# Kernel tuning notes

Hardware: AMD Instinct MI355X
Metric: run time of the kernel (lower is better)

Reference implementation:

```python
import jax, jax.numpy as jnp
import numpy as np

B, T, C, H = 4, 2048, 1024, 16


def setup_inputs() -> dict:
    key = jax.random.key(0)
    ks = jax.random.split(key, 8)
    s = 0.02
    return {
        "xq": jax.random.normal(ks[0], (B, T, C), jnp.float32),
        "xk": jax.random.normal(ks[1], (B, T, C), jnp.float32),
        "xv": jax.random.normal(ks[2], (B, T, C), jnp.float32),
        "Wq": jax.random.normal(ks[3], (C, C), jnp.float32) * s,
        "Wk": jax.random.normal(ks[4], (C, C), jnp.float32) * s,
        "Wv": jax.random.normal(ks[5], (C, C), jnp.float32) * s,
        "Wo": jax.random.normal(ks[6], (C, C), jnp.float32) * s,
        "bo": jnp.zeros((C,), jnp.float32),
    }


def reference(xq, xk, xv, Wq, Wk, Wv, Wo, bo):
    # torch nn.Linear: y = x @ W.T
    q = xq @ Wq.T  # (B,T,C)
    k = xk @ Wk.T
    v = xv @ Wv.T
    hd = C // H
    # (B,T,C) -> (B,H,T,hd)
    q = q.reshape(B, T, H, hd).transpose(0, 2, 1, 3)
    k = k.reshape(B, T, H, hd).transpose(0, 2, 1, 3)
    v = v.reshape(B, T, H, hd).transpose(0, 2, 1, 3)
    scale = 1.0 / jnp.sqrt(jnp.asarray(hd, q.dtype))
    att = jnp.einsum("bhqd,bhkd->bhqk", q, k) * scale  # (B,H,T,T)
    causal = jnp.tril(jnp.ones((T, T), bool))
    att = jnp.where(causal, att, jnp.asarray(-jnp.inf, att.dtype))
    att = jax.nn.softmax(att, axis=-1)
    y = jnp.einsum("bhqk,bhkd->bhqd", att, v)  # (B,H,T,hd)
    y = y.transpose(0, 2, 1, 3).reshape(B, T, C)
    return y @ Wo.T + bo
```

## Files before the change

### kernel.cpp

```cpp
#include <hip/hip_runtime.h>
#include <stdint.h>

#define B_ 4
#define T_ 2048
#define C_ 1024
#define H_ 16
#define HD 64

typedef __attribute__((ext_vector_type(8))) short bf16x8;
typedef __attribute__((ext_vector_type(4))) short bf16x4;
typedef __attribute__((ext_vector_type(4))) float v4f;
typedef __attribute__((ext_vector_type(4))) uint32_t v4u;

static __device__ __forceinline__ short f2bf(float f) {
    union { float f; uint32_t u; } v; v.f = f;
    uint32_t u = v.u;
    uint32_t r = (u + 0x7fffu + ((u >> 16) & 1u)) >> 16;
    return (short)(r & 0xffffu);
}
static __device__ __forceinline__ uint32_t pack2(float x, float y) {
    uint32_t a = __float_as_uint(x) + 0x8000u;
    uint32_t b = __float_as_uint(y) + 0x8000u;
    return __builtin_amdgcn_perm(b, a, 0x07060302u);
}
static __device__ __forceinline__ uint32_t pack2t(float x, float y) {
    return __builtin_amdgcn_perm(__float_as_uint(y), __float_as_uint(x), 0x07060302u);
}
static __device__ __forceinline__ void gload_lds16(const void* g, void* l) {
    __builtin_amdgcn_global_load_lds(
        (const __attribute__((address_space(1))) void*)g,
        (__attribute__((address_space(3))) void*)l, 16, 0, 0);
}

__global__ __launch_bounds__(256) void convw(
    const float* __restrict__ w0, const float* __restrict__ w1,
    const float* __restrict__ w2, const float* __restrict__ w3,
    short* __restrict__ out)
{
    const float* src = (blockIdx.y == 0) ? w0 : (blockIdx.y == 1) ? w1 :
                       (blockIdx.y == 2) ? w2 : w3;
    short* dst = out + (size_t)blockIdx.y * (C_ * C_);
    int id = blockIdx.x * 256 + threadIdx.x;
    const float* p = src + (size_t)id * 8;
    v4f a0 = *(const v4f*)p, a1 = *(const v4f*)(p + 4);
    v4u dv;
    dv[0] = pack2(a0[0], a0[1]); dv[1] = pack2(a0[2], a0[3]);
    dv[2] = pack2(a1[0], a1[1]); dv[3] = pack2(a1[2], a1[3]);
    *(v4u*)&dst[(size_t)id * 8] = dv;
}

template <int MODE>
__global__ __launch_bounds__(256) void gemm_nt(
    const void* A0, const void* A1,
    const void* B0, const void* B1,
    void* O0, void* O1,
    const float* __restrict__ bias, float s0, float s1)
{
    const void* Aptr = blockIdx.z ? A1 : A0;
    const void* Bptr = blockIdx.z ? B1 : B0;
    void* Out = blockIdx.z ? O1 : O0;
    const float oscale = blockIdx.z ? s1 : s0;

    const int K = 1024;
    __shared__ short As[128 * 32];
    __shared__ short Bs[128 * 32];
    const int t = threadIdx.x;
    const int w = t >> 6, l = t & 63, g = l >> 4, c = l & 15;
    const int wm = w & 1, wn = w >> 1;
    const int m0 = blockIdx.x * 128, n0 = blockIdx.y * 128;

    v4f acc[4][4];
#pragma unroll
    for (int i = 0; i < 4; ++i)
#pragma unroll
        for (int j = 0; j < 4; ++j) acc[i][j] = (v4f){0.f, 0.f, 0.f, 0.f};

    for (int k0 = 0; k0 < K; k0 += 32) {
        __syncthreads();
        if (MODE != 0) {
            const short* Ab = (const short*)Aptr;
#pragma unroll
            for (int i = 0; i < 2; ++i) {
                int cb = w * 2 + i;
                const short* gp = Ab + (size_t)(m0 + cb * 16 + (l >> 2)) * K + k0 + (l & 3) * 8;
                gload_lds16(gp, &As[cb * 512]);
            }
        }
        if (MODE != 1) {
            const short* Bb = (const short*)Bptr;
#pragma unroll
            for (int i = 0; i < 2; ++i) {
                int cb = w * 2 + i;
                const short* gp = Bb + (size_t)(n0 + cb * 16 + (l >> 2)) * K + k0 + (l & 3) * 8;
                gload_lds16(gp, &Bs[cb * 512]);
            }
        }
        if (MODE == 0) {
            const float* Af = (const float*)Aptr;
#pragma unroll
            for (int i = 0; i < 2; ++i) {
                int id = i * 256 + t;
                const float* p = Af + (size_t)(m0 + (id >> 2)) * K + k0 + (id & 3) * 8;
                v4f a0 = *(const v4f*)p, a1 = *(const v4f*)(p + 4);
                v4u dv;
                dv[0] = pack2(a0[0], a0[1]); dv[1] = pack2(a0[2], a0[3]);
                dv[2] = pack2(a1[0], a1[1]); dv[3] = pack2(a1[2], a1[3]);
                *(v4u*)&As[id * 8] = dv;
            }
        }
        if (MODE == 1) {
            const float* Bf = (const float*)Bptr;
#pragma unroll
            for (int i = 0; i < 2; ++i) {
                int id = i * 256 + t;
                const float* p = Bf + (size_t)(n0 + (id >> 2)) * K + k0 + (id & 3) * 8;
                v4f a0 = *(const v4f*)p, a1 = *(const v4f*)(p + 4);
                v4u dv;
                dv[0] = pack2(a0[0], a0[1]); dv[1] = pack2(a0[2], a0[3]);
                dv[2] = pack2(a1[0], a1[1]); dv[3] = pack2(a1[2], a1[3]);
                *(v4u*)&Bs[id * 8] = dv;
            }
        }
        __syncthreads();
        bf16x8 af[4], bfr[4];
#pragma unroll
        for (int i = 0; i < 4; ++i)
            af[i] = *(const bf16x8*)&As[(wm * 64 + i * 16 + c) * 32 + g * 8];
#pragma unroll
        for (int j = 0; j < 4; ++j)
            bfr[j] = *(const bf16x8*)&Bs[(wn * 64 + j * 16 + c) * 32 + g * 8];
#pragma unroll
        for (int i = 0; i < 4; ++i)
#pragma unroll
            for (int j = 0; j < 4; ++j)
                acc[i][j] = __builtin_amdgcn_mfma_f32_16x16x32_bf16(af[i], bfr[j], acc[i][j], 0, 0, 0);
    }
#pragma unroll
    for (int i = 0; i < 4; ++i)
#pragma unroll
        for (int j = 0; j < 4; ++j)
#pragma unroll
            for (int r = 0; r < 4; ++r) {
                int m = m0 + wm * 64 + i * 16 + g * 4 + r;
                int n = n0 + wn * 64 + j * 16 + c;
                float vv = acc[i][j][r];
                if (MODE == 2) {
                    ((float*)Out)[(size_t)m * C_ + n] = vv + bias[n];
                } else if (MODE == 0) {
                    int b = m >> 11, tt = m & (T_ - 1);
                    int h = n >> 6, d = n & 63;
                    ((short*)Out)[((size_t)(b * H_ + h) * T_ + tt) * HD + d] = f2bf(vv * oscale);
                } else {
                    int b = n >> 11, tt = n & (T_ - 1);
                    int h = m >> 6, d = m & 63;
                    ((short*)Out)[((size_t)(b * H_ + h) * HD + d) * T_ + tt] = f2bf(vv);
                }
            }
}

__global__ __launch_bounds__(256) void attn_kernel(
    const short* __restrict__ Q, const short* __restrict__ Kp,
    const short* __restrict__ Vt, short* __restrict__ Y)
{
    __shared__ short Ks[2 * 64 * 32];
    __shared__ short Vs[64 * 72];
    const int t = threadIdx.x;
    const int w = t >> 6, l = t & 63, g = l >> 4, c = l & 15;
    const int bid = blockIdx.x;
    const int slot = bid >> 3;
    const int p = slot & 15;
    const size_t bh = (size_t)((bid & 7) * 8 + (slot >> 4));

    bf16x8 ones;
#pragma unroll
    for (int i = 0; i < 8; ++i) ones[i] = (short)0x3F80;

    for (int qi = 0; qi < 2; ++qi) {
        const int qt = qi ? (31 - p) : p;
        const int qbase = qt * 64;

        bf16x8 qf0, qf1;
        {
            const short* qp = &Q[(bh * T_ + qbase + w * 16 + c) * HD + g * 8];
            qf0 = *(const bf16x8*)qp;
            qf1 = *(const bf16x8*)(qp + 32);
        }

        v4f O[4], accl;
        accl = (v4f){0.f, 0.f, 0.f, 0.f};
#pragma unroll
        for (int d = 0; d < 4; ++d) O[d] = (v4f){0.f, 0.f, 0.f, 0.f};

        for (int kb = 0; kb <= qt; ++kb) {
            const int kbase = kb * 64;
            __syncthreads();
#pragma unroll
            for (int i = 0; i < 2; ++i) {
                int gi = w * 2 + i;
                int hk = gi >> 2, rb = gi & 3;
                const short* gp = &Kp[(bh * T_ + kbase + rb * 16 + (l >> 2)) * HD + hk * 32 + (l & 3) * 8];
                gload_lds16(gp, &Ks[hk * 2048 + rb * 512]);
            }
#pragma unroll
            for (int i = 0; i < 2; ++i) {
                int id = i * 256 + t;
                int rr = id >> 3, cc = id & 7;
                *(bf16x8*)&Vs[rr * 72 + cc * 8] =
                    *(const bf16x8*)&Vt[(bh * HD + rr) * T_ + kbase + cc * 8];
            }
            __syncthreads();

            float s2[4][4];
#pragma unroll
            for (int j = 0; j < 4; ++j) {
                bf16x8 kf0 = *(const bf16x8*)&Ks[(j * 16 + c) * 32 + g * 8];
                bf16x8 kf1 = *(const bf16x8*)&Ks[2048 + (j * 16 + c) * 32 + g * 8];
                v4f sa = (v4f){0.f, 0.f, 0.f, 0.f};
                sa = __builtin_amdgcn_mfma_f32_16x16x32_bf16(kf0, qf0, sa, 0, 0, 0);
                sa = __builtin_amdgcn_mfma_f32_16x16x32_bf16(kf1, qf1, sa, 0, 0, 0);
#pragma unroll
                for (int r = 0; r < 4; ++r) s2[j][r] = sa[r];
            }
            if (kb == qt) {
                const int q = qbase + w * 16 + c;
#pragma unroll
                for (int j = 0; j < 4; ++j)
#pragma unroll
                    for (int r = 0; r < 4; ++r) {
                        int key = kbase + j * 16 + g * 4 + r;
                        if (key > q) s2[j][r] = -3.0e38f;
                    }
            }
            union { bf16x8 v; uint32_t u[4]; } pa[2];
#pragma unroll
            for (int s = 0; s < 2; ++s)
#pragma unroll
                for (int wi = 0; wi < 4; ++wi) {
                    int j = 2 * s + (wi >> 1);
                    int r0 = (wi & 1) * 2;
                    float x = __builtin_amdgcn_exp2f(s2[j][r0]);
                    float y = __builtin_amdgcn_exp2f(s2[j][r0 + 1]);
                    pa[s].u[wi] = pack2t(x, y);
                }
#pragma unroll
            for (int s = 0; s < 2; ++s) {
                bf16x8 af = pa[s].v;
#pragma unroll
                for (int d = 0; d < 4; ++d) {
                    const short* vp = &Vs[(d * 16 + c) * 72 + s * 32 + g * 4];
                    union { bf16x8 v8; bf16x4 v4[2]; } vu;
                    vu.v4[0] = *(const bf16x4*)vp;
                    vu.v4[1] = *(const bf16x4*)(vp + 16);
                    O[d] = __builtin_amdgcn_mfma_f32_16x16x32_bf16(af, vu.v8, O[d], 0, 0, 0);
                }
                accl = __builtin_amdgcn_mfma_f32_16x16x32_bf16(af, ones, accl, 0, 0, 0);
            }
        }
#pragma unroll
        for (int r = 0; r < 4; ++r) {
            float rl = 1.0f / accl[r];
            size_t rowoff = ((size_t)(bh >> 4) * T_ + qbase + w * 16 + g * 4 + r) * C_ + (bh & 15) * HD;
#pragma unroll
            for (int d = 0; d < 4; ++d)
                Y[rowoff + d * 16 + c] = f2bf(O[d][r] * rl);
        }
    }
}

extern "C" void kernel_launch(void* const* d_in, const int* in_sizes, int n_in,
                              void* d_out, int out_size, void* d_ws, size_t ws_size,
                              hipStream_t stream) {
    const float* xq = (const float*)d_in[0];
    const float* xk = (const float*)d_in[1];
    const float* xv = (const float*)d_in[2];
    const float* Wq = (const float*)d_in[3];
    const float* Wk = (const float*)d_in[4];
    const float* Wv = (const float*)d_in[5];
    const float* Wo = (const float*)d_in[6];
    const float* bo = (const float*)d_in[7];

    const size_t NE = (size_t)B_ * H_ * T_ * HD;
    const size_t WE = (size_t)C_ * C_;
    short* Qh  = (short*)d_ws;
    short* Kh  = Qh + NE;
    short* Vt  = Kh + NE;
    short* Y   = Vt + NE;
    short* Wbf = Y + NE;

    const float qscale = 0.18033688011112042f;
    dim3 blk(256);

    hipLaunchKernelGGL(convw, dim3(512, 4), blk, 0, stream, Wq, Wk, Wv, Wo, Wbf);
    hipLaunchKernelGGL((gemm_nt<0>), dim3(64, 8, 2), blk, 0, stream,
                       (const void*)xq, (const void*)xk,
                       (const void*)(Wbf + 0 * WE), (const void*)(Wbf + 1 * WE),
                       (void*)Qh, (void*)Kh, (const float*)nullptr, qscale, 1.0f);
    hipLaunchKernelGGL((gemm_nt<1>), dim3(8, 64, 1), blk, 0, stream,
                       (const void*)(Wbf + 2 * WE), (const void*)(Wbf + 2 * WE),
                       (const void*)xv, (const void*)xv,
                       (void*)Vt, (void*)Vt, (const float*)nullptr, 1.0f, 1.0f);
    hipLaunchKernelGGL(attn_kernel, dim3(B_ * H_ * (T_ / 128)), blk, 0, stream, Qh, Kh, Vt, Y);
    hipLaunchKernelGGL((gemm_nt<2>), dim3(64, 8, 1), blk, 0, stream,
                       (const void*)Y, (const void*)Y,
                       (const void*)(Wbf + 3 * WE), (const void*)(Wbf + 3 * WE),
                       d_out, d_out, bo, 1.0f, 1.0f);
}
```

Baseline: 362.4 us.

## Swizzle LDS tiles, pre-convert inputs to bf16, merge QKV projections into one launch

Adds an XOR swizzle to LDS tile layouts in all GEMMs and the attention K tile to remove bank conflicts on fragment reads. Converts xq/xk to bf16 in a separate pass together with the weights, so projection GEMMs can use direct global-to-LDS loads. Merges the Q, K and V projections into one three-slice launch and stores Vt in the output buffer as scratch. The trade-off is extra memory traffic for the conversion pass.

```diff
diff --git a/kernel.cpp b/kernel.cpp
--- a/kernel.cpp
+++ b/kernel.cpp
@@ -32,35 +32,140 @@
         (__attribute__((address_space(3))) void*)l, 16, 0, 0);
 }
 
-__global__ __launch_bounds__(256) void convw(
+__global__ __launch_bounds__(256) void convx(
+    const float* __restrict__ x0, const float* __restrict__ x1,
+    short* __restrict__ o0, short* __restrict__ o1,
     const float* __restrict__ w0, const float* __restrict__ w1,
     const float* __restrict__ w2, const float* __restrict__ w3,
-    short* __restrict__ out)
+    short* __restrict__ wout)
 {
-    const float* src = (blockIdx.y == 0) ? w0 : (blockIdx.y == 1) ? w1 :
-                       (blockIdx.y == 2) ? w2 : w3;
-    short* dst = out + (size_t)blockIdx.y * (C_ * C_);
-    int id = blockIdx.x * 256 + threadIdx.x;
-    const float* p = src + (size_t)id * 8;
+    int bid = blockIdx.x;
+    const float* src; short* dst; size_t id;
+    if (bid < 8192) {
+        src = (bid < 4096) ? x0 : x1;
+        dst = (bid < 4096) ? o0 : o1;
+        id = (size_t)(bid & 4095) * 256 + threadIdx.x;
+    } else {
+        int wb = bid - 8192;
+        int wi = wb >> 9;
+        src = (wi == 0) ? w0 : (wi == 1) ? w1 : (wi == 2) ? w2 : w3;
+        dst = wout + (size_t)wi * (C_ * C_);
+        id = (size_t)(wb & 511) * 256 + threadIdx.x;
+    }
+    const float* p = src + id * 8;
     v4f a0 = *(const v4f*)p, a1 = *(const v4f*)(p + 4);
     v4u dv;
     dv[0] = pack2(a0[0], a0[1]); dv[1] = pack2(a0[2], a0[3]);
     dv[2] = pack2(a1[0], a1[1]); dv[3] = pack2(a1[2], a1[3]);
-    *(v4u*)&dst[(size_t)id * 8] = dv;
-}
-
-template <int MODE>
-__global__ __launch_bounds__(256) void gemm_nt(
-    const void* A0, const void* A1,
-    const void* B0, const void* B1,
-    void* O0, void* O1,
-    const float* __restrict__ bias, float s0, float s1)
+    *(v4u*)&dst[id * 8] = dv;
+}
+
+
+__global__ __launch_bounds__(256) void proj_gemm(
+    const short* __restrict__ Xq, const short* __restrict__ Xk,
+    const short* __restrict__ Wb, const float* __restrict__ xv,
+    short* __restrict__ Qh, short* __restrict__ Kh, short* __restrict__ Vt,
+    float qscale)
 {
-    const void* Aptr = blockIdx.z ? A1 : A0;
-    const void* Bptr = blockIdx.z ? B1 : B0;
-    void* Out = blockIdx.z ? O1 : O0;
-    const float oscale = blockIdx.z ? s1 : s0;
-
+    const int K = 1024;
+    __shared__ short As[128 * 32];
+    __shared__ short Bs[128 * 32];
+    const int t = threadIdx.x;
+    const int w = t >> 6, l = t & 63, g = l >> 4, c = l & 15;
+    const int wm = w & 1, wn = w >> 1;
+    const int z = blockIdx.z;
+    const int m0 = (z == 2 ? blockIdx.y : blockIdx.x) * 128;
+    const int n0 = (z == 2 ? blockIdx.x : blockIdx.y) * 128;
+    const short* Ab = (z == 0) ? Xq : (z == 1) ? Xk : (Wb + 2 * C_ * C_);
+    const short* Bb = (z == 0) ? Wb : (Wb + C_ * C_);
+
+    const int srow = l >> 2;
+    const int sch = (l & 3) ^ ((l >> 3) & 3);
+    const int gs = (g ^ ((c >> 1) & 3)) * 8;
+
+    v4f acc[4][4];
+#pragma unroll
+    for (int i = 0; i < 4; ++i)
+#pragma unroll
+        for (int j = 0; j < 4; ++j) acc[i][j] = (v4f){0.f, 0.f, 0.f, 0.f};
+
+    for (int k0 = 0; k0 < K; k0 += 32) {
+        __syncthreads();
+#pragma unroll
+        for (int i = 0; i < 2; ++i) {
+            int cb = w * 2 + i;
+            gload_lds16(Ab + (size_t)(m0 + cb * 16 + srow) * K + k0 + sch * 8,
+                        &As[cb * 512]);
+        }
+        if (z < 2) {
+#pragma unroll
+            for (int i = 0; i < 2; ++i) {
+                int cb = w * 2 + i;
+                gload_lds16(Bb + (size_t)(n0 + cb * 16 + srow) * K + k0 + sch * 8,
+                            &Bs[cb * 512]);
+            }
+        } else {
+#pragma unroll
+            for (int i = 0; i < 2; ++i) {
+                int id = i * 256 + t;
+                int rr = id >> 2, cc = id & 3;
+                const float* p = xv + (size_t)(n0 + rr) * K + k0 + cc * 8;
+                v4f a0 = *(const v4f*)p, a1 = *(const v4f*)(p + 4);
+                v4u dv;
+                dv[0] = pack2(a0[0], a0[1]); dv[1] = pack2(a0[2], a0[3]);
+                dv[2] = pack2(a1[0], a1[1]); dv[3] = pack2(a1[2], a1[3]);
+                *(v4u*)&Bs[rr * 32 + ((cc ^ ((rr >> 1) & 3)) * 8)] = dv;
+            }
+        }
+        __syncthreads();
+        bf16x8 af[4], bfr[4];
+#pragma unroll
+        for (int i = 0; i < 4; ++i)
+            af[i] = *(const bf16x8*)&As[(wm * 64 + i * 16 + c) * 32 + gs];
+#pragma unroll
+        for (int j = 0; j < 4; ++j)
+            bfr[j] = *(const bf16x8*)&Bs[(wn * 64 + j * 16 + c) * 32 + gs];
+#pragma unroll
+        for (int i = 0; i < 4; ++i)
+#pragma unroll
+            for (int j = 0; j < 4; ++j)
+                acc[i][j] = __builtin_amdgcn_mfma_f32_16x16x32_bf16(af[i], bfr[j], acc[i][j], 0, 0, 0);
+    }
+    if (z < 2) {
+        short* Out = (z == 0) ? Qh : Kh;
+        const float os = (z == 0) ? qscale : 1.0f;
+#pragma unroll
+        for (int i = 0; i < 4; ++i)
+#pragma unroll
+            for (int j = 0; j < 4; ++j)
+#pragma unroll
+                for (int r = 0; r < 4; ++r) {
+                    int m = m0 + wm * 64 + i * 16 + g * 4 + r;
+                    int n = n0 + wn * 64 + j * 16 + c;
+                    int b = m >> 11, tt = m & (T_ - 1);
+                    int h = n >> 6, d = n & 63;
+                    Out[((size_t)(b * H_ + h) * T_ + tt) * HD + d] = f2bf(acc[i][j][r] * os);
+                }
+    } else {
+#pragma unroll
+        for (int i = 0; i < 4; ++i)
+#pragma unroll
+            for (int j = 0; j < 4; ++j)
+#pragma unroll
+                for (int r = 0; r < 4; ++r) {
+                    int m = m0 + wm * 64 + i * 16 + g * 4 + r;
+                    int n = n0 + wn * 64 + j * 16 + c;
+                    int b = n >> 11, tt = n & (T_ - 1);
+                    int h = m >> 6, d = m & 63;
+                    Vt[((size_t)(b * H_ + h) * HD + d) * T_ + tt] = f2bf(acc[i][j][r]);
+                }
+    }
+}
+
+__global__ __launch_bounds__(256) void gemm_o(
+    const short* __restrict__ Yb, const short* __restrict__ Wo,
+    float* __restrict__ Out, const float* __restrict__ bias)
+{
     const int K = 1024;
     __shared__ short As[128 * 32];
     __shared__ short Bs[128 * 32];
@@ -69,6 +174,10 @@
     const int wm = w & 1, wn = w >> 1;
     const int m0 = blockIdx.x * 128, n0 = blockIdx.y * 128;
 
+    const int srow = l >> 2;
+    const int sch = (l & 3) ^ ((l >> 3) & 3);
+    const int gs = (g ^ ((c >> 1) & 3)) * 8;
+
     v4f acc[4][4];
 #pragma unroll
     for (int i = 0; i < 4; ++i)
@@ -77,58 +186,22 @@
 
     for (int k0 = 0; k0 < K; k0 += 32) {
         __syncthreads();
-        if (MODE != 0) {
-            const short* Ab = (const short*)Aptr;
-#pragma unroll
-            for (int i = 0; i < 2; ++i) {
-                int cb = w * 2 + i;
-                const short* gp = Ab + (size_t)(m0 + cb * 16 + (l >> 2)) * K + k0 + (l & 3) * 8;
-                gload_lds16(gp, &As[cb * 512]);
-            }
-        }
-        if (MODE != 1) {
-            const short* Bb = (const short*)Bptr;
-#pragma unroll
-            for (int i = 0; i < 2; ++i) {
-                int cb = w * 2 + i;
-                const short* gp = Bb + (size_t)(n0 + cb * 16 + (l >> 2)) * K + k0 + (l & 3) * 8;
-                gload_lds16(gp, &Bs[cb * 512]);
-            }
-        }
-        if (MODE == 0) {
-            const float* Af = (const float*)Aptr;
-#pragma unroll
-            for (int i = 0; i < 2; ++i) {
-                int id = i * 256 + t;
-                const float* p = Af + (size_t)(m0 + (id >> 2)) * K + k0 + (id & 3) * 8;
-                v4f a0 = *(const v4f*)p, a1 = *(const v4f*)(p + 4);
-                v4u dv;
-                dv[0] = pack2(a0[0], a0[1]); dv[1] = pack2(a0[2], a0[3]);
-                dv[2] = pack2(a1[0], a1[1]); dv[3] = pack2(a1[2], a1[3]);
-                *(v4u*)&As[id * 8] = dv;
-            }
-        }
-        if (MODE == 1) {
-            const float* Bf = (const float*)Bptr;
-#pragma unroll
-            for (int i = 0; i < 2; ++i) {
-                int id = i * 256 + t;
-                const float* p = Bf + (size_t)(n0 + (id >> 2)) * K + k0 + (id & 3) * 8;
-                v4f a0 = *(const v4f*)p, a1 = *(const v4f*)(p + 4);
-                v4u dv;
-                dv[0] = pack2(a0[0], a0[1]); dv[1] = pack2(a0[2], a0[3]);
-                dv[2] = pack2(a1[0], a1[1]); dv[3] = pack2(a1[2], a1[3]);
-                *(v4u*)&Bs[id * 8] = dv;
-            }
+#pragma unroll
+        for (int i = 0; i < 2; ++i) {
+            int cb = w * 2 + i;
+            gload_lds16(Yb + (size_t)(m0 + cb * 16 + srow) * K + k0 + sch * 8,
+                        &As[cb * 512]);
+            gload_lds16(Wo + (size_t)(n0 + cb * 16 + srow) * K + k0 + sch * 8,
+                        &Bs[cb * 512]);
         }
         __syncthreads();
         bf16x8 af[4], bfr[4];
 #pragma unroll
         for (int i = 0; i < 4; ++i)
-            af[i] = *(const bf16x8*)&As[(wm * 64 + i * 16 + c) * 32 + g * 8];
+            af[i] = *(const bf16x8*)&As[(wm * 64 + i * 16 + c) * 32 + gs];
 #pragma unroll
         for (int j = 0; j < 4; ++j)
-            bfr[j] = *(const bf16x8*)&Bs[(wn * 64 + j * 16 + c) * 32 + g * 8];
+            bfr[j] = *(const bf16x8*)&Bs[(wn * 64 + j * 16 + c) * 32 + gs];
 #pragma unroll
         for (int i = 0; i < 4; ++i)
 #pragma unroll
@@ -143,18 +216,7 @@
             for (int r = 0; r < 4; ++r) {
                 int m = m0 + wm * 64 + i * 16 + g * 4 + r;
                 int n = n0 + wn * 64 + j * 16 + c;
-                float vv = acc[i][j][r];
-                if (MODE == 2) {
-                    ((float*)Out)[(size_t)m * C_ + n] = vv + bias[n];
-                } else if (MODE == 0) {
-                    int b = m >> 11, tt = m & (T_ - 1);
-                    int h = n >> 6, d = n & 63;
-                    ((short*)Out)[((size_t)(b * H_ + h) * T_ + tt) * HD + d] = f2bf(vv * oscale);
-                } else {
-                    int b = n >> 11, tt = n & (T_ - 1);
-                    int h = m >> 6, d = m & 63;
-                    ((short*)Out)[((size_t)(b * H_ + h) * HD + d) * T_ + tt] = f2bf(vv);
-                }
+                Out[(size_t)m * C_ + n] = acc[i][j][r] + bias[n];
             }
 }
 
@@ -171,6 +233,10 @@
     const int p = slot & 15;
     const size_t bh = (size_t)((bid & 7) * 8 + (slot >> 4));
 
+    const int srow = l >> 2;
+    const int sch = (l & 3) ^ ((l >> 3) & 3);
+    const int gs = (g ^ ((c >> 1) & 3)) * 8;
+
     bf16x8 ones;
 #pragma unroll
     for (int i = 0; i < 8; ++i) ones[i] = (short)0x3F80;
@@ -198,7 +264,7 @@
             for (int i = 0; i < 2; ++i) {
                 int gi = w * 2 + i;
                 int hk = gi >> 2, rb = gi & 3;
-                const short* gp = &Kp[(bh * T_ + kbase + rb * 16 + (l >> 2)) * HD + hk * 32 + (l & 3) * 8];
+                const short* gp = &Kp[(bh * T_ + kbase + rb * 16 + srow) * HD + hk * 32 + sch * 8];
                 gload_lds16(gp, &Ks[hk * 2048 + rb * 512]);
             }
 #pragma unroll
@@ -213,8 +279,8 @@
             float s2[4][4];
 #pragma unroll
             for (int j = 0; j < 4; ++j) {
-                bf16x8 kf0 = *(const bf16x8*)&Ks[(j * 16 + c) * 32 + g * 8];
-                bf16x8 kf1 = *(const bf16x8*)&Ks[2048 + (j * 16 + c) * 32 + g * 8];
+                bf16x8 kf0 = *(const bf16x8*)&Ks[(j * 16 + c) * 32 + gs];
+                bf16x8 kf1 = *(const bf16x8*)&Ks[2048 + (j * 16 + c) * 32 + gs];
                 v4f sa = (v4f){0.f, 0.f, 0.f, 0.f};
                 sa = __builtin_amdgcn_mfma_f32_16x16x32_bf16(kf0, qf0, sa, 0, 0, 0);
                 sa = __builtin_amdgcn_mfma_f32_16x16x32_bf16(kf1, qf1, sa, 0, 0, 0);
@@ -281,27 +347,22 @@
 
     const size_t NE = (size_t)B_ * H_ * T_ * HD;
     const size_t WE = (size_t)C_ * C_;
-    short* Qh  = (short*)d_ws;
-    short* Kh  = Qh + NE;
-    short* Vt  = Kh + NE;
-    short* Y   = Vt + NE;
-    short* Wbf = Y + NE;
+    short* Qh    = (short*)d_ws;
+    short* Kh    = Qh + NE;
+    short* slotA = Kh + NE;
+    short* slotB = slotA + NE;
+    short* Wbf   = slotB + NE;
+    short* Vt    = (short*)d_out;
 
     const float qscale = 0.18033688011112042f;
     dim3 blk(256);
 
-    hipLaunchKernelGGL(convw, dim3(512, 4), blk, 0, stream, Wq, Wk, Wv, Wo, Wbf);
-    hipLaunchKernelGGL((gemm_nt<0>), dim3(64, 8, 2), blk, 0, stream,
-                       (const void*)xq, (const void*)xk,
-                       (const void*)(Wbf + 0 * WE), (const void*)(Wbf + 1 * WE),
-                       (void*)Qh, (void*)Kh, (const float*)nullptr, qscale, 1.0f);
-    hipLaunchKernelGGL((gemm_nt<1>), dim3(8, 64, 1), blk, 0, stream,
-                       (const void*)(Wbf + 2 * WE), (const void*)(Wbf + 2 * WE),
-                       (const void*)xv, (const void*)xv,
-                       (void*)Vt, (void*)Vt, (const float*)nullptr, 1.0f, 1.0f);
-    hipLaunchKernelGGL(attn_kernel, dim3(B_ * H_ * (T_ / 128)), blk, 0, stream, Qh, Kh, Vt, Y);
-    hipLaunchKernelGGL((gemm_nt<2>), dim3(64, 8, 1), blk, 0, stream,
-                       (const void*)Y, (const void*)Y,
-                       (const void*)(Wbf + 3 * WE), (const void*)(Wbf + 3 * WE),
-                       d_out, d_out, bo, 1.0f, 1.0f);
-}
+    hipLaunchKernelGGL(convx, dim3(10240), blk, 0, stream,
+                       xq, xk, slotA, slotB, Wq, Wk, Wv, Wo, Wbf);
+    hipLaunchKernelGGL(proj_gemm, dim3(64, 8, 3), blk, 0, stream,
+                       slotA, slotB, Wbf, xv, Qh, Kh, Vt, qscale);
+    hipLaunchKernelGGL(attn_kernel, dim3(B_ * H_ * (T_ / 128)), blk, 0, stream,
+                       Qh, Kh, Vt, slotA);
+    hipLaunchKernelGGL(gemm_o, dim3(64, 8), blk, 0, stream,
+                       slotA, Wbf + 3 * WE, (float*)d_out, bo);
+}
```

Measured after the change: 323.5 us. -10.7%, faster.
